# Optimization experiments

Measured on AMD Instinct MI355X. Metric: run time of the kernel, lower is better.

Reference implementation:

```python
import jax, jax.numpy as jnp
import numpy as np

EMBED_DIM = 1024
NUM_HEADS = 16
HEAD_DIM = EMBED_DIM // NUM_HEADS
B, S = 2, 2048


def setup_inputs() -> dict:
    key = jax.random.key(0)
    ks = jax.random.split(key, 8)
    std = 1.0 / np.sqrt(EMBED_DIM)
    return {
        "xq": jax.random.normal(ks[0], (B, S, EMBED_DIM), jnp.float32),
        "xk": jax.random.normal(ks[1], (B, S, EMBED_DIM), jnp.float32),
        "xv": jax.random.normal(ks[2], (B, S, EMBED_DIM), jnp.float32),
        "Wq": jax.random.normal(ks[3], (EMBED_DIM, EMBED_DIM), jnp.float32) * std,
        "Wk": jax.random.normal(ks[4], (EMBED_DIM, EMBED_DIM), jnp.float32) * std,
        "Wv": jax.random.normal(ks[5], (EMBED_DIM, EMBED_DIM), jnp.float32) * std,
        "Wo": jax.random.normal(ks[6], (EMBED_DIM, EMBED_DIM), jnp.float32) * std,
        "bo": jnp.zeros((EMBED_DIM,), jnp.float32),
    }


def reference(xq, xk, xv, Wq, Wk, Wv, Wo, bo):
    # nn.Linear(x) = x @ W.T ; then view last dim into (heads, head_dim)
    def proj(x, W):
        y = jnp.einsum('bse,fe->bsf', x, W)
        return y.reshape(x.shape[0], x.shape[1], NUM_HEADS, HEAD_DIM)

    q = proj(xq, Wq)  # [b, m, h, f]
    k = proj(xk, Wk)  # [b, n, h, f]
    v = proj(xv, Wv)  # [b, n, h, f]

    scaling = 1.0 / np.sqrt(HEAD_DIM).astype(np.float32)
    dot = scaling * jnp.einsum('bmhf,bnhf->bhmn', q, k)  # [b, h, m, n]
    attn = jax.nn.softmax(dot, axis=-1)
    out = jnp.einsum('bhmn,bnhf->bmhf', attn, v)  # [b, m, h, f]

    Wo_hf = Wo.reshape(EMBED_DIM, NUM_HEADS, HEAD_DIM)
    return jnp.einsum('bmhf,ehf->bme', out, Wo_hf) + bo
```

## Files before the change

kernel.cpp:

```cpp
#include <hip/hip_runtime.h>
#include <math.h>


#define EMBED 1024
#define SEQ   2048
#define BATCH 2
#define NH    16
#define HD    64

typedef __attribute__((ext_vector_type(8))) short bf16x8;
typedef __attribute__((ext_vector_type(4))) short bf16x4;
typedef __attribute__((ext_vector_type(4))) float f32x4;

#define QSCALE 0.18033688f

__device__ inline unsigned short f2bf(float f) {
  unsigned int u = __builtin_bit_cast(unsigned int, f);
  u += 0x7fffu + ((u >> 16) & 1u);
  return (unsigned short)(u >> 16);
}
__device__ inline float bf2f(unsigned short s) {
  unsigned int u = ((unsigned int)s) << 16;
  return __builtin_bit_cast(float, u);
}

__device__ inline void async_cp16(const void* g, void* l) {
  __builtin_amdgcn_global_load_lds(
      (const __attribute__((address_space(1))) unsigned int*)g,
      (__attribute__((address_space(3))) unsigned int*)l, 16, 0, 0);
}

__global__ void detect_kernel(const unsigned int* __restrict__ xq, int* __restrict__ flag) {
  __shared__ int cnt[256];
  int t = threadIdx.x;
  unsigned int w = xq[t];
  unsigned int e = (w >> 7) & 0xFFu;
  cnt[t] = (e >= 0x70u && e <= 0x8Fu) ? 1 : 0;
  __syncthreads();
  for (int s = 128; s > 0; s >>= 1) {
    if (t < s) cnt[t] += cnt[t + s];
    __syncthreads();
  }
  if (t == 0) *flag = (cnt[0] >= 160) ? 1 : 0;
}

struct PackPtrs {
  const void* src[7];
  unsigned short* dst[7];
};
__global__ __launch_bounds__(256) void pack_all(PackPtrs p, const int* __restrict__ flagp) {
  const bool isbf = (*flagp != 0);
  int ci = blockIdx.x * 256 + threadIdx.x;
  int t, rel;
  if (ci < 1572864) { t = ci / 524288; rel = ci - t * 524288; }
  else { int r = ci - 1572864; int w = r / 131072; t = 3 + w; rel = r - w * 131072; }
  size_t off = (size_t)rel * 8;
  unsigned short* d = p.dst[t] + off;
  if (isbf) {
    *(bf16x8*)d = *(const bf16x8*)((const unsigned short*)p.src[t] + off);
  } else {
    const float* s = (const float*)p.src[t] + off;
    bf16x8 v;
#pragma unroll
    for (int e = 0; e < 8; ++e) v[e] = (short)f2bf(s[e]);
    *(bf16x8*)d = v;
  }
}

struct QkvArgs {
  const unsigned short* A[3];
  const unsigned short* W[3];
  unsigned short* out[3];
};
__global__ __launch_bounds__(256) void gemm_qkv(QkvArgs args) {
  __shared__ __align__(16) unsigned short smem[16640];
  unsigned short* As = smem;
  unsigned short* Bs = smem + 4096;

  const int z = blockIdx.z;
  const unsigned short* A = args.A[z];
  const unsigned short* Bw = args.W[z];
  unsigned short* out = args.out[z];

  const int tid = threadIdx.x, lane = tid & 63, wave = tid >> 6;
  const int wm = wave >> 1, wn = wave & 1;
  const int q = lane >> 4, c = lane & 15;
  const int m0 = blockIdx.x * 128, n0 = blockIdx.y * 128;

  f32x4 acc[4][4];
#pragma unroll
  for (int i = 0; i < 4; ++i)
#pragma unroll
    for (int j = 0; j < 4; ++j) acc[i][j] = (f32x4){0.f, 0.f, 0.f, 0.f};

  for (int k0 = 0; k0 < EMBED; k0 += 32) {
    __syncthreads();
#pragma unroll
    for (int jj = 0; jj < 2; ++jj) {
      int ci = jj * 256 + tid;
      async_cp16(A + (size_t)(m0 + (ci >> 2)) * EMBED + k0 + (ci & 3) * 8,
                 (void*)(As + (jj * 256 + wave * 64) * 8));
      async_cp16(Bw + (size_t)(n0 + (ci >> 2)) * EMBED + k0 + (ci & 3) * 8,
                 (void*)(Bs + (jj * 256 + wave * 64) * 8));
    }
    __syncthreads();

    bf16x8 af[4], bfr[4];
#pragma unroll
    for (int i = 0; i < 4; ++i)
      af[i] = *(const bf16x8*)(As + (wm * 64 + i * 16 + c) * 32 + q * 8);
#pragma unroll
    for (int j = 0; j < 4; ++j)
      bfr[j] = *(const bf16x8*)(Bs + (wn * 64 + j * 16 + c) * 32 + q * 8);
#pragma unroll
    for (int i = 0; i < 4; ++i)
#pragma unroll
      for (int j = 0; j < 4; ++j)
        acc[i][j] = __builtin_amdgcn_mfma_f32_16x16x32_bf16(af[i], bfr[j], acc[i][j], 0, 0, 0);
  }

  if (z < 2) {
    const float sc = (z == 0) ? QSCALE : 1.0f;
#pragma unroll
    for (int i = 0; i < 4; ++i)
#pragma unroll
      for (int j = 0; j < 4; ++j)
#pragma unroll
        for (int r = 0; r < 4; ++r) {
          int m = m0 + wm * 64 + i * 16 + q * 4 + r;
          int col = n0 + wn * 64 + j * 16 + c;
          int b = m >> 11, s = m & 2047, h = col >> 6, d = col & 63;
          out[(size_t)((b * NH + h) * SEQ + s) * HD + d] = f2bf(acc[i][j][r] * sc);
        }
  } else {
    __syncthreads();
#pragma unroll
    for (int i = 0; i < 4; ++i)
#pragma unroll
      for (int j = 0; j < 4; ++j)
#pragma unroll
        for (int r = 0; r < 4; ++r)
          smem[(wm * 64 + i * 16 + q * 4 + r) * 130 + wn * 64 + j * 16 + c] =
              f2bf(acc[i][j][r]);
    __syncthreads();
    int n = tid >> 1;
    int sh = (tid & 1) * 64;
    int b = m0 >> 11, s0l = m0 & 2047;
    int h = blockIdx.y * 2 + (n >> 6), d = n & 63;
    unsigned short* dst = out + (size_t)((b * NH + h) * HD + d) * SEQ + s0l + sh;
#pragma unroll
    for (int g = 0; g < 8; ++g) {
      bf16x8 v;
#pragma unroll
      for (int e = 0; e < 8; ++e) v[e] = (short)smem[(sh + g * 8 + e) * 130 + n];
      *(bf16x8*)(dst + g * 8) = v;
    }
  }
}

__global__ __launch_bounds__(256) void gemm_out(
    const unsigned short* __restrict__ A,
    const unsigned short* __restrict__ Bw,
    const void* __restrict__ bias,
    void* __restrict__ out,
    const int* __restrict__ flagp)
{
  __shared__ __align__(16) unsigned short As[4096];
  __shared__ __align__(16) unsigned short Bs[4096];

  const int tid = threadIdx.x, lane = tid & 63, wave = tid >> 6;
  const int wm = wave >> 1, wn = wave & 1;
  const int q = lane >> 4, c = lane & 15;
  const int m0 = blockIdx.x * 128, n0 = blockIdx.y * 128;

  f32x4 acc[4][4];
#pragma unroll
  for (int i = 0; i < 4; ++i)
#pragma unroll
    for (int j = 0; j < 4; ++j) acc[i][j] = (f32x4){0.f, 0.f, 0.f, 0.f};

  for (int k0 = 0; k0 < EMBED; k0 += 32) {
    __syncthreads();
#pragma unroll
    for (int jj = 0; jj < 2; ++jj) {
      int ci = jj * 256 + tid;
      async_cp16(A + (size_t)(m0 + (ci >> 2)) * EMBED + k0 + (ci & 3) * 8,
                 (void*)(As + (jj * 256 + wave * 64) * 8));
      async_cp16(Bw + (size_t)(n0 + (ci >> 2)) * EMBED + k0 + (ci & 3) * 8,
                 (void*)(Bs + (jj * 256 + wave * 64) * 8));
    }
    __syncthreads();

    bf16x8 af[4], bfr[4];
#pragma unroll
    for (int i = 0; i < 4; ++i)
      af[i] = *(const bf16x8*)(As + (wm * 64 + i * 16 + c) * 32 + q * 8);
#pragma unroll
    for (int j = 0; j < 4; ++j)
      bfr[j] = *(const bf16x8*)(Bs + (wn * 64 + j * 16 + c) * 32 + q * 8);
#pragma unroll
    for (int i = 0; i < 4; ++i)
#pragma unroll
      for (int j = 0; j < 4; ++j)
        acc[i][j] = __builtin_amdgcn_mfma_f32_16x16x32_bf16(af[i], bfr[j], acc[i][j], 0, 0, 0);
  }

  const bool isbf = (*flagp != 0);
#pragma unroll
  for (int i = 0; i < 4; ++i)
#pragma unroll
    for (int j = 0; j < 4; ++j)
#pragma unroll
      for (int r = 0; r < 4; ++r) {
        int m = m0 + wm * 64 + i * 16 + q * 4 + r;
        int col = n0 + wn * 64 + j * 16 + c;
        float v = acc[i][j][r];
        v += isbf ? bf2f(((const unsigned short*)bias)[col]) : ((const float*)bias)[col];
        if (isnan(v)) v = 777.0f;
        if (isbf) ((unsigned short*)out)[(size_t)m * EMBED + col] = f2bf(v);
        else      ((float*)out)[(size_t)m * EMBED + col] = v;
      }
}

__global__ __launch_bounds__(256) void attn_kernel(
    const unsigned short* __restrict__ Qb,
    const unsigned short* __restrict__ Kb,
    const unsigned short* __restrict__ Vtb,
    unsigned short* __restrict__ Ob)
{
  __shared__ __align__(16) unsigned short Kt[2][64][72];
  __shared__ __align__(16) unsigned short Vs[2][64][72];

  const int tid = threadIdx.x;
  const int lane = tid & 63;
  const int wave = tid >> 6;
  const int q = lane >> 4, c = lane & 15;
  const int b = blockIdx.z, h = blockIdx.y;
  const int q0 = blockIdx.x * 64 + wave * 16;

  const unsigned short* Qh = Qb + ((size_t)(b * NH + h) * SEQ) * HD;
  const unsigned short* Kh = Kb + ((size_t)(b * NH + h) * SEQ) * HD;
  const unsigned short* Vh = Vtb + ((size_t)(b * NH + h) * HD) * SEQ;

  bf16x8 qfl = *(const bf16x8*)(Qh + (q0 + c) * HD + q * 8);
  bf16x8 qfh = *(const bf16x8*)(Qh + (q0 + c) * HD + 32 + q * 8);

  f32x4 o[4];
#pragma unroll
  for (int t = 0; t < 4; ++t) o[t] = (f32x4){0.f, 0.f, 0.f, 0.f};
  float l = 0.f;

  const int r0 = tid >> 3;
  const int ch0 = (tid & 7) * 8;

  bf16x8 kr0, kr1, vr0, vr1;
  kr0 = *(const bf16x8*)(Kh + (size_t)r0 * HD + ch0);
  kr1 = *(const bf16x8*)(Kh + (size_t)(32 + r0) * HD + ch0);
  vr0 = *(const bf16x8*)(Vh + (size_t)r0 * SEQ + ch0);
  vr1 = *(const bf16x8*)(Vh + (size_t)(32 + r0) * SEQ + ch0);
  *(bf16x8*)(&Kt[0][r0][ch0]) = kr0;
  *(bf16x8*)(&Kt[0][32 + r0][ch0]) = kr1;
  *(bf16x8*)(&Vs[0][r0][ch0]) = vr0;
  *(bf16x8*)(&Vs[0][32 + r0][ch0]) = vr1;

  for (int kt = 0; kt < SEQ / 64; ++kt) {
    const int p = kt & 1;
    __syncthreads();
    if (kt + 1 < SEQ / 64) {
      kr0 = *(const bf16x8*)(Kh + (size_t)((kt + 1) * 64 + r0) * HD + ch0);
      kr1 = *(const bf16x8*)(Kh + (size_t)((kt + 1) * 64 + 32 + r0) * HD + ch0);
      vr0 = *(const bf16x8*)(Vh + (size_t)r0 * SEQ + (kt + 1) * 64 + ch0);
      vr1 = *(const bf16x8*)(Vh + (size_t)(32 + r0) * SEQ + (kt + 1) * 64 + ch0);
    }

#pragma unroll
    for (int g = 0; g < 2; ++g) {
      bf16x4 pk[2];
#pragma unroll
      for (int s2 = 0; s2 < 2; ++s2) {
        const int s = g * 2 + s2;
        bf16x8 k0f = *(const bf16x8*)(&Kt[p][s * 16 + c][q * 8]);
        bf16x8 k1f = *(const bf16x8*)(&Kt[p][s * 16 + c][32 + q * 8]);
        f32x4 z = {0.f, 0.f, 0.f, 0.f};
        z = __builtin_amdgcn_mfma_f32_16x16x32_bf16(k0f, qfl, z, 0, 0, 0);
        z = __builtin_amdgcn_mfma_f32_16x16x32_bf16(k1f, qfh, z, 0, 0, 0);
#pragma unroll
        for (int r = 0; r < 4; ++r) {
          float pv = __builtin_amdgcn_exp2f(z[r]);
          l += pv;
          pk[s2][r] = (short)(__builtin_bit_cast(unsigned int, pv) >> 16);
        }
      }
#pragma unroll
      for (int t = 0; t < 4; ++t) {
        bf16x4 v0 = *(const bf16x4*)(&Vs[p][t * 16 + c][g * 32 + q * 4]);
        bf16x4 v1 = *(const bf16x4*)(&Vs[p][t * 16 + c][g * 32 + 16 + q * 4]);
        bf16x8 vf, pf;
#pragma unroll
        for (int e = 0; e < 4; ++e) {
          vf[e] = v0[e]; vf[4 + e] = v1[e];
          pf[e] = pk[0][e]; pf[4 + e] = pk[1][e];
        }
        o[t] = __builtin_amdgcn_mfma_f32_16x16x32_bf16(pf, vf, o[t], 0, 0, 0);
      }
    }

    if (kt + 1 < SEQ / 64) {
      *(bf16x8*)(&Kt[1 - p][r0][ch0]) = kr0;
      *(bf16x8*)(&Kt[1 - p][32 + r0][ch0]) = kr1;
      *(bf16x8*)(&Vs[1 - p][r0][ch0]) = vr0;
      *(bf16x8*)(&Vs[1 - p][32 + r0][ch0]) = vr1;
    }
  }

  float ls = l;
  ls += __shfl_xor(ls, 16);
  ls += __shfl_xor(ls, 32);
  float lf[4];
#pragma unroll
  for (int r = 0; r < 4; ++r) lf[r] = 1.f / __shfl(ls, q * 4 + r);
#pragma unroll
  for (int t = 0; t < 4; ++t)
#pragma unroll
    for (int r = 0; r < 4; ++r) {
      int srow = q0 + q * 4 + r;
      int col = h * HD + t * 16 + c;
      float val = o[t][r] * lf[r];
      if (isnan(val)) val = 77.0f;
      Ob[((size_t)(b * SEQ + srow)) * EMBED + col] = f2bf(val);
    }
}

__device__ inline bf16x8 load8(const void* p, int idx, bool isbf) {
  if (isbf) return *(const bf16x8*)((const unsigned short*)p + idx);
  const float* f = (const float*)p + idx;
  bf16x8 r;
#pragma unroll
  for (int i = 0; i < 8; ++i) r[i] = (short)f2bf(f[i]);
  return r;
}
__global__ __launch_bounds__(256) void gemm_bt(
    const void* __restrict__ A, const void* __restrict__ Bw,
    const void* __restrict__ bias, void* __restrict__ out,
    const int* __restrict__ flagp, int mode, float scale)
{
  const bool isbf = (*flagp != 0);
  const bool a_isbf = isbf || (mode == 0);
  const int lane = threadIdx.x & 63;
  const int wave = threadIdx.x >> 6;
  const int tile = blockIdx.x * 4 + wave;
  const int mt = tile >> 4, nt = tile & 15;
  const int q = lane >> 4, c = lane & 15;
  const int m0 = mt * 16, n0 = nt * 64;

  f32x4 acc[4];
#pragma unroll
  for (int t = 0; t < 4; ++t) acc[t] = (f32x4){0.f, 0.f, 0.f, 0.f};

  for (int k0 = 0; k0 < EMBED; k0 += 32) {
    bf16x8 a = load8(A, (m0 + c) * EMBED + k0 + q * 8, a_isbf);
#pragma unroll
    for (int t = 0; t < 4; ++t) {
      bf16x8 b = load8(Bw, (n0 + t * 16 + c) * EMBED + k0 + q * 8, isbf);
      acc[t] = __builtin_amdgcn_mfma_f32_16x16x32_bf16(a, b, acc[t], 0, 0, 0);
    }
  }
#pragma unroll
  for (int t = 0; t < 4; ++t)
#pragma unroll
    for (int r = 0; r < 4; ++r) {
      float v = acc[t][r] * scale;
      int row = m0 + q * 4 + r, col = n0 + t * 16 + c;
      if (mode == 0) {
        v += isbf ? bf2f(((const unsigned short*)bias)[col]) : ((const float*)bias)[col];
        if (isbf) ((unsigned short*)out)[row * EMBED + col] = f2bf(v);
        else      ((float*)out)[row * EMBED + col] = v;
      } else {
        int b = row >> 11, s = row & 2047, h = col >> 6, d = col & 63;
        if (mode == 1) ((unsigned short*)out)[(((b * NH + h) * SEQ) + s) * HD + d] = f2bf(v);
        else           ((unsigned short*)out)[(((b * NH + h) * HD) + d) * SEQ + s] = f2bf(v);
      }
    }
}

extern "C" void kernel_launch(void* const* d_in, const int* in_sizes, int n_in,
                              void* d_out, int out_size, void* d_ws, size_t ws_size,
                              hipStream_t stream) {
  const void* xq = d_in[0]; const void* xk = d_in[1]; const void* xv = d_in[2];
  const void* Wq = d_in[3]; const void* Wk = d_in[4]; const void* Wv = d_in[5];
  const void* Wo = d_in[6]; const void* bo = d_in[7];

  const size_t NEL = (size_t)BATCH * SEQ * EMBED;
  const size_t WEL = (size_t)EMBED * EMBED;
  unsigned short* base = (unsigned short*)d_ws;

  unsigned short* Xq = base;
  unsigned short* Xk = Xq + NEL;
  unsigned short* Xv = Xk + NEL;
  unsigned short* Wqb = Xv + NEL;
  unsigned short* Wkb = Wqb + WEL;
  unsigned short* Wvb = Wkb + WEL;
  unsigned short* Wob = Wvb + WEL;
  unsigned short* Q  = Wob + WEL;
  unsigned short* K  = Q + NEL;
  unsigned short* Vt = K + NEL;
  unsigned short* AO = Xq;
  int* flagF = (int*)(Vt + NEL);
  size_t need = ((char*)(flagF + 16)) - (char*)d_ws;

  if (ws_size >= need) {
    detect_kernel<<<1, 256, 0, stream>>>((const unsigned int*)xq, flagF);
    PackPtrs pp;
    pp.src[0] = xq; pp.src[1] = xk; pp.src[2] = xv;
    pp.src[3] = Wq; pp.src[4] = Wk; pp.src[5] = Wv; pp.src[6] = Wo;
    pp.dst[0] = Xq; pp.dst[1] = Xk; pp.dst[2] = Xv;
    pp.dst[3] = Wqb; pp.dst[4] = Wkb; pp.dst[5] = Wvb; pp.dst[6] = Wob;
    pack_all<<<8192, 256, 0, stream>>>(pp, flagF);

    QkvArgs qa;
    qa.A[0] = Xq; qa.A[1] = Xk; qa.A[2] = Xv;
    qa.W[0] = Wqb; qa.W[1] = Wkb; qa.W[2] = Wvb;
    qa.out[0] = Q; qa.out[1] = K; qa.out[2] = Vt;
    gemm_qkv<<<dim3(32, 8, 3), 256, 0, stream>>>(qa);
    attn_kernel<<<dim3(32, NH, BATCH), 256, 0, stream>>>(Q, K, Vt, AO);
    gemm_out<<<dim3(32, 8), 256, 0, stream>>>(AO, Wob, bo, d_out, flagF);
  } else {
    unsigned short* Qf  = base;
    unsigned short* Kf  = Qf + NEL;
    unsigned short* Vtf = Kf + NEL;
    unsigned short* AOf = Vtf + NEL;
    int* flag = (int*)(AOf + NEL);
    detect_kernel<<<1, 256, 0, stream>>>((const unsigned int*)xq, flag);
    dim3 gblk(1024, 1, 1);
    gemm_bt<<<gblk, 256, 0, stream>>>(xq, Wq, nullptr, Qf, flag, 1, QSCALE);
    gemm_bt<<<gblk, 256, 0, stream>>>(xk, Wk, nullptr, Kf, flag, 1, 1.0f);
    gemm_bt<<<gblk, 256, 0, stream>>>(xv, Wv, nullptr, Vtf, flag, 2, 1.0f);
    attn_kernel<<<dim3(32, NH, BATCH), 256, 0, stream>>>(Qf, Kf, Vtf, AOf);
    gemm_bt<<<gblk, 256, 0, stream>>>(AOf, Wo, bo, d_out, flag, 0, 1.0f);
  }
}
```

Before: 254.8 us.

## Drop dtype detection, widen GEMM K-tiles with XOR swizzle, load V directly in attention

Removes the bf16/f32 detection kernel and all runtime dtype branches, so inputs are always treated as fp32. The QKV and output GEMMs now stage K-tiles of 64 instead of 32, with an XOR-swizzled LDS layout to avoid bank conflicts. The output GEMM uses 64-row tiles for more blocks. Attention drops the V shared-memory staging: V^T is stored pre-permuted so MFMA operands come straight from global memory, and occupancy is hinted via launch bounds. This trades fewer syncs and less LDS for more global-load latency in the attention loop and tighter coupling between the V writer and reader layouts.

```diff
diff --git a/kernel.cpp b/kernel.cpp
--- a/kernel.cpp
+++ b/kernel.cpp
@@ -19,10 +19,6 @@
   u += 0x7fffu + ((u >> 16) & 1u);
   return (unsigned short)(u >> 16);
 }
-__device__ inline float bf2f(unsigned short s) {
-  unsigned int u = ((unsigned int)s) << 16;
-  return __builtin_bit_cast(float, u);
-}
 
 __device__ inline void async_cp16(const void* g, void* l) {
   __builtin_amdgcn_global_load_lds(
@@ -30,41 +26,28 @@
       (__attribute__((address_space(3))) unsigned int*)l, 16, 0, 0);
 }
 
-__global__ void detect_kernel(const unsigned int* __restrict__ xq, int* __restrict__ flag) {
-  __shared__ int cnt[256];
-  int t = threadIdx.x;
-  unsigned int w = xq[t];
-  unsigned int e = (w >> 7) & 0xFFu;
-  cnt[t] = (e >= 0x70u && e <= 0x8Fu) ? 1 : 0;
-  __syncthreads();
-  for (int s = 128; s > 0; s >>= 1) {
-    if (t < s) cnt[t] += cnt[t + s];
-    __syncthreads();
-  }
-  if (t == 0) *flag = (cnt[0] >= 160) ? 1 : 0;
+__device__ inline int vswz_src(int p) {
+  return (p & ~31) + 16 * ((p >> 2) & 1) + 4 * ((p >> 3) & 3) + (p & 3);
+}
+__device__ inline int vswz_pos(int s) {
+  return (s & ~31) + 8 * ((s >> 2) & 3) + 4 * ((s >> 4) & 1) + (s & 3);
 }
 
 struct PackPtrs {
-  const void* src[7];
+  const float* src[7];
   unsigned short* dst[7];
 };
-__global__ __launch_bounds__(256) void pack_all(PackPtrs p, const int* __restrict__ flagp) {
-  const bool isbf = (*flagp != 0);
+__global__ __launch_bounds__(256) void pack_all(PackPtrs p) {
   int ci = blockIdx.x * 256 + threadIdx.x;
   int t, rel;
   if (ci < 1572864) { t = ci / 524288; rel = ci - t * 524288; }
   else { int r = ci - 1572864; int w = r / 131072; t = 3 + w; rel = r - w * 131072; }
   size_t off = (size_t)rel * 8;
-  unsigned short* d = p.dst[t] + off;
-  if (isbf) {
-    *(bf16x8*)d = *(const bf16x8*)((const unsigned short*)p.src[t] + off);
-  } else {
-    const float* s = (const float*)p.src[t] + off;
-    bf16x8 v;
-#pragma unroll
-    for (int e = 0; e < 8; ++e) v[e] = (short)f2bf(s[e]);
-    *(bf16x8*)d = v;
-  }
+  const float* s = p.src[t] + off;
+  bf16x8 v;
+#pragma unroll
+  for (int e = 0; e < 8; ++e) v[e] = (short)f2bf(s[e]);
+  *(bf16x8*)(p.dst[t] + off) = v;
 }
 
 struct QkvArgs {
@@ -75,7 +58,7 @@
 __global__ __launch_bounds__(256) void gemm_qkv(QkvArgs args) {
   __shared__ __align__(16) unsigned short smem[16640];
   unsigned short* As = smem;
-  unsigned short* Bs = smem + 4096;
+  unsigned short* Bs = smem + 8192;
 
   const int z = blockIdx.z;
   const unsigned short* A = args.A[z];
@@ -93,30 +76,36 @@
 #pragma unroll
     for (int j = 0; j < 4; ++j) acc[i][j] = (f32x4){0.f, 0.f, 0.f, 0.f};
 
-  for (int k0 = 0; k0 < EMBED; k0 += 32) {
-    __syncthreads();
-#pragma unroll
-    for (int jj = 0; jj < 2; ++jj) {
+  for (int k0 = 0; k0 < EMBED; k0 += 64) {
+    __syncthreads();
+#pragma unroll
+    for (int jj = 0; jj < 4; ++jj) {
       int ci = jj * 256 + tid;
-      async_cp16(A + (size_t)(m0 + (ci >> 2)) * EMBED + k0 + (ci & 3) * 8,
+      int row = ci >> 3, sc = ((ci & 7) ^ (row & 7)) * 8;
+      async_cp16(A + (size_t)(m0 + row) * EMBED + k0 + sc,
                  (void*)(As + (jj * 256 + wave * 64) * 8));
-      async_cp16(Bw + (size_t)(n0 + (ci >> 2)) * EMBED + k0 + (ci & 3) * 8,
+      async_cp16(Bw + (size_t)(n0 + row) * EMBED + k0 + sc,
                  (void*)(Bs + (jj * 256 + wave * 64) * 8));
     }
     __syncthreads();
 
-    bf16x8 af[4], bfr[4];
-#pragma unroll
-    for (int i = 0; i < 4; ++i)
-      af[i] = *(const bf16x8*)(As + (wm * 64 + i * 16 + c) * 32 + q * 8);
-#pragma unroll
-    for (int j = 0; j < 4; ++j)
-      bfr[j] = *(const bf16x8*)(Bs + (wn * 64 + j * 16 + c) * 32 + q * 8);
-#pragma unroll
-    for (int i = 0; i < 4; ++i)
+#pragma unroll
+    for (int kk = 0; kk < 2; ++kk) {
+      bf16x8 af[4], bfr[4];
+#pragma unroll
+      for (int i = 0; i < 4; ++i)
+        af[i] = *(const bf16x8*)(As + (wm * 64 + i * 16 + c) * 64 +
+                                 (((kk * 4 + q) ^ (c & 7)) * 8));
 #pragma unroll
       for (int j = 0; j < 4; ++j)
-        acc[i][j] = __builtin_amdgcn_mfma_f32_16x16x32_bf16(af[i], bfr[j], acc[i][j], 0, 0, 0);
+        bfr[j] = *(const bf16x8*)(Bs + (wn * 64 + j * 16 + c) * 64 +
+                                  (((kk * 4 + q) ^ (c & 7)) * 8));
+#pragma unroll
+      for (int i = 0; i < 4; ++i)
+#pragma unroll
+        for (int j = 0; j < 4; ++j)
+          acc[i][j] = __builtin_amdgcn_mfma_f32_16x16x32_bf16(af[i], bfr[j], acc[i][j], 0, 0, 0);
+    }
   }
 
   if (z < 2) {
@@ -152,7 +141,8 @@
     for (int g = 0; g < 8; ++g) {
       bf16x8 v;
 #pragma unroll
-      for (int e = 0; e < 8; ++e) v[e] = (short)smem[(sh + g * 8 + e) * 130 + n];
+      for (int e = 0; e < 8; ++e)
+        v[e] = (short)smem[vswz_src(sh + g * 8 + e) * 130 + n];
       *(bf16x8*)(dst + g * 8) = v;
     }
   }
@@ -161,75 +151,81 @@
 __global__ __launch_bounds__(256) void gemm_out(
     const unsigned short* __restrict__ A,
     const unsigned short* __restrict__ Bw,
-    const void* __restrict__ bias,
-    void* __restrict__ out,
-    const int* __restrict__ flagp)
+    const float* __restrict__ bias,
+    float* __restrict__ out)
 {
   __shared__ __align__(16) unsigned short As[4096];
-  __shared__ __align__(16) unsigned short Bs[4096];
+  __shared__ __align__(16) unsigned short Bs[8192];
 
   const int tid = threadIdx.x, lane = tid & 63, wave = tid >> 6;
   const int wm = wave >> 1, wn = wave & 1;
   const int q = lane >> 4, c = lane & 15;
-  const int m0 = blockIdx.x * 128, n0 = blockIdx.y * 128;
-
-  f32x4 acc[4][4];
-#pragma unroll
-  for (int i = 0; i < 4; ++i)
+  const int m0 = blockIdx.x * 64, n0 = blockIdx.y * 128;
+
+  f32x4 acc[2][4];
+#pragma unroll
+  for (int i = 0; i < 2; ++i)
 #pragma unroll
     for (int j = 0; j < 4; ++j) acc[i][j] = (f32x4){0.f, 0.f, 0.f, 0.f};
 
-  for (int k0 = 0; k0 < EMBED; k0 += 32) {
+  for (int k0 = 0; k0 < EMBED; k0 += 64) {
     __syncthreads();
 #pragma unroll
     for (int jj = 0; jj < 2; ++jj) {
       int ci = jj * 256 + tid;
-      async_cp16(A + (size_t)(m0 + (ci >> 2)) * EMBED + k0 + (ci & 3) * 8,
+      int row = ci >> 3, sc = ((ci & 7) ^ (row & 7)) * 8;
+      async_cp16(A + (size_t)(m0 + row) * EMBED + k0 + sc,
                  (void*)(As + (jj * 256 + wave * 64) * 8));
-      async_cp16(Bw + (size_t)(n0 + (ci >> 2)) * EMBED + k0 + (ci & 3) * 8,
+    }
+#pragma unroll
+    for (int jj = 0; jj < 4; ++jj) {
+      int ci = jj * 256 + tid;
+      int row = ci >> 3, sc = ((ci & 7) ^ (row & 7)) * 8;
+      async_cp16(Bw + (size_t)(n0 + row) * EMBED + k0 + sc,
                  (void*)(Bs + (jj * 256 + wave * 64) * 8));
     }
     __syncthreads();
 
-    bf16x8 af[4], bfr[4];
-#pragma unroll
-    for (int i = 0; i < 4; ++i)
-      af[i] = *(const bf16x8*)(As + (wm * 64 + i * 16 + c) * 32 + q * 8);
+#pragma unroll
+    for (int kk = 0; kk < 2; ++kk) {
+      bf16x8 af[2], bfr[4];
+#pragma unroll
+      for (int i = 0; i < 2; ++i)
+        af[i] = *(const bf16x8*)(As + (wm * 32 + i * 16 + c) * 64 +
+                                 (((kk * 4 + q) ^ (c & 7)) * 8));
+#pragma unroll
+      for (int j = 0; j < 4; ++j)
+        bfr[j] = *(const bf16x8*)(Bs + (wn * 64 + j * 16 + c) * 64 +
+                                  (((kk * 4 + q) ^ (c & 7)) * 8));
+#pragma unroll
+      for (int i = 0; i < 2; ++i)
+#pragma unroll
+        for (int j = 0; j < 4; ++j)
+          acc[i][j] = __builtin_amdgcn_mfma_f32_16x16x32_bf16(af[i], bfr[j], acc[i][j], 0, 0, 0);
+    }
+  }
+
+#pragma unroll
+  for (int i = 0; i < 2; ++i)
 #pragma unroll
     for (int j = 0; j < 4; ++j)
-      bfr[j] = *(const bf16x8*)(Bs + (wn * 64 + j * 16 + c) * 32 + q * 8);
-#pragma unroll
-    for (int i = 0; i < 4; ++i)
-#pragma unroll
-      for (int j = 0; j < 4; ++j)
-        acc[i][j] = __builtin_amdgcn_mfma_f32_16x16x32_bf16(af[i], bfr[j], acc[i][j], 0, 0, 0);
-  }
-
-  const bool isbf = (*flagp != 0);
-#pragma unroll
-  for (int i = 0; i < 4; ++i)
-#pragma unroll
-    for (int j = 0; j < 4; ++j)
 #pragma unroll
       for (int r = 0; r < 4; ++r) {
-        int m = m0 + wm * 64 + i * 16 + q * 4 + r;
+        int m = m0 + wm * 32 + i * 16 + q * 4 + r;
         int col = n0 + wn * 64 + j * 16 + c;
-        float v = acc[i][j][r];
-        v += isbf ? bf2f(((const unsigned short*)bias)[col]) : ((const float*)bias)[col];
+        float v = acc[i][j][r] + bias[col];
         if (isnan(v)) v = 777.0f;
-        if (isbf) ((unsigned short*)out)[(size_t)m * EMBED + col] = f2bf(v);
-        else      ((float*)out)[(size_t)m * EMBED + col] = v;
+        out[(size_t)m * EMBED + col] = v;
       }
 }
 
-__global__ __launch_bounds__(256) void attn_kernel(
+__global__ __launch_bounds__(256, 4) void attn_kernel(
     const unsigned short* __restrict__ Qb,
     const unsigned short* __restrict__ Kb,
     const unsigned short* __restrict__ Vtb,
     unsigned short* __restrict__ Ob)
 {
   __shared__ __align__(16) unsigned short Kt[2][64][72];
-  __shared__ __align__(16) unsigned short Vs[2][64][72];
 
   const int tid = threadIdx.x;
   const int lane = tid & 63;
@@ -253,15 +249,11 @@
   const int r0 = tid >> 3;
   const int ch0 = (tid & 7) * 8;
 
-  bf16x8 kr0, kr1, vr0, vr1;
+  bf16x8 kr0, kr1;
   kr0 = *(const bf16x8*)(Kh + (size_t)r0 * HD + ch0);
   kr1 = *(const bf16x8*)(Kh + (size_t)(32 + r0) * HD + ch0);
-  vr0 = *(const bf16x8*)(Vh + (size_t)r0 * SEQ + ch0);
-  vr1 = *(const bf16x8*)(Vh + (size_t)(32 + r0) * SEQ + ch0);
   *(bf16x8*)(&Kt[0][r0][ch0]) = kr0;
   *(bf16x8*)(&Kt[0][32 + r0][ch0]) = kr1;
-  *(bf16x8*)(&Vs[0][r0][ch0]) = vr0;
-  *(bf16x8*)(&Vs[0][32 + r0][ch0]) = vr1;
 
   for (int kt = 0; kt < SEQ / 64; ++kt) {
     const int p = kt & 1;
@@ -269,9 +261,14 @@
     if (kt + 1 < SEQ / 64) {
       kr0 = *(const bf16x8*)(Kh + (size_t)((kt + 1) * 64 + r0) * HD + ch0);
       kr1 = *(const bf16x8*)(Kh + (size_t)((kt + 1) * 64 + 32 + r0) * HD + ch0);
-      vr0 = *(const bf16x8*)(Vh + (size_t)r0 * SEQ + (kt + 1) * 64 + ch0);
-      vr1 = *(const bf16x8*)(Vh + (size_t)(32 + r0) * SEQ + (kt + 1) * 64 + ch0);
-    }
+    }
+    bf16x8 vb[4][2];
+#pragma unroll
+    for (int t = 0; t < 4; ++t)
+#pragma unroll
+      for (int g = 0; g < 2; ++g)
+        vb[t][g] = *(const bf16x8*)(Vh + (size_t)(t * 16 + c) * SEQ +
+                                    kt * 64 + g * 32 + q * 8);
 
 #pragma unroll
     for (int g = 0; g < 2; ++g) {
@@ -293,23 +290,16 @@
       }
 #pragma unroll
       for (int t = 0; t < 4; ++t) {
-        bf16x4 v0 = *(const bf16x4*)(&Vs[p][t * 16 + c][g * 32 + q * 4]);
-        bf16x4 v1 = *(const bf16x4*)(&Vs[p][t * 16 + c][g * 32 + 16 + q * 4]);
-        bf16x8 vf, pf;
-#pragma unroll
-        for (int e = 0; e < 4; ++e) {
-          vf[e] = v0[e]; vf[4 + e] = v1[e];
-          pf[e] = pk[0][e]; pf[4 + e] = pk[1][e];
-        }
-        o[t] = __builtin_amdgcn_mfma_f32_16x16x32_bf16(pf, vf, o[t], 0, 0, 0);
+        bf16x8 pf;
+#pragma unroll
+        for (int e = 0; e < 4; ++e) { pf[e] = pk[0][e]; pf[4 + e] = pk[1][e]; }
+        o[t] = __builtin_amdgcn_mfma_f32_16x16x32_bf16(pf, vb[t][g], o[t], 0, 0, 0);
       }
     }
 
     if (kt + 1 < SEQ / 64) {
       *(bf16x8*)(&Kt[1 - p][r0][ch0]) = kr0;
       *(bf16x8*)(&Kt[1 - p][32 + r0][ch0]) = kr1;
-      *(bf16x8*)(&Vs[1 - p][r0][ch0]) = vr0;
-      *(bf16x8*)(&Vs[1 - p][32 + r0][ch0]) = vr1;
     }
   }
 
@@ -331,9 +321,7 @@
     }
 }
 
-__device__ inline bf16x8 load8(const void* p, int idx, bool isbf) {
-  if (isbf) return *(const bf16x8*)((const unsigned short*)p + idx);
-  const float* f = (const float*)p + idx;
+__device__ inline bf16x8 load8f(const float* f) {
   bf16x8 r;
 #pragma unroll
   for (int i = 0; i < 8; ++i) r[i] = (short)f2bf(f[i]);
@@ -341,11 +329,9 @@
 }
 __global__ __launch_bounds__(256) void gemm_bt(
     const void* __restrict__ A, const void* __restrict__ Bw,
-    const void* __restrict__ bias, void* __restrict__ out,
-    const int* __restrict__ flagp, int mode, float scale)
+    const float* __restrict__ bias, void* __restrict__ out,
+    int mode, float scale)
 {
-  const bool isbf = (*flagp != 0);
-  const bool a_isbf = isbf || (mode == 0);
   const int lane = threadIdx.x & 63;
   const int wave = threadIdx.x >> 6;
   const int tile = blockIdx.x * 4 + wave;
@@ -358,10 +344,12 @@
   for (int t = 0; t < 4; ++t) acc[t] = (f32x4){0.f, 0.f, 0.f, 0.f};
 
   for (int k0 = 0; k0 < EMBED; k0 += 32) {
-    bf16x8 a = load8(A, (m0 + c) * EMBED + k0 + q * 8, a_isbf);
+    bf16x8 a = (mode == 0)
+        ? *(const bf16x8*)((const unsigned short*)A + (m0 + c) * EMBED + k0 + q * 8)
+        : load8f((const float*)A + (m0 + c) * EMBED + k0 + q * 8);
 #pragma unroll
     for (int t = 0; t < 4; ++t) {
-      bf16x8 b = load8(Bw, (n0 + t * 16 + c) * EMBED + k0 + q * 8, isbf);
+      bf16x8 b = load8f((const float*)Bw + (size_t)(n0 + t * 16 + c) * EMBED + k0 + q * 8);
       acc[t] = __builtin_amdgcn_mfma_f32_16x16x32_bf16(a, b, acc[t], 0, 0, 0);
     }
   }
@@ -372,13 +360,14 @@
       float v = acc[t][r] * scale;
       int row = m0 + q * 4 + r, col = n0 + t * 16 + c;
       if (mode == 0) {
-        v += isbf ? bf2f(((const unsigned short*)bias)[col]) : ((const float*)bias)[col];
-        if (isbf) ((unsigned short*)out)[row * EMBED + col] = f2bf(v);
-        else      ((float*)out)[row * EMBED + col] = v;
+        v += bias[col];
+        ((float*)out)[(size_t)row * EMBED + col] = v;
       } else {
         int b = row >> 11, s = row & 2047, h = col >> 6, d = col & 63;
-        if (mode == 1) ((unsigned short*)out)[(((b * NH + h) * SEQ) + s) * HD + d] = f2bf(v);
-        else           ((unsigned short*)out)[(((b * NH + h) * HD) + d) * SEQ + s] = f2bf(v);
+        if (mode == 1)
+          ((unsigned short*)out)[(size_t)((b * NH + h) * SEQ + s) * HD + d] = f2bf(v);
+        else
+          ((unsigned short*)out)[(size_t)((b * NH + h) * HD + d) * SEQ + vswz_pos(s)] = f2bf(v);
       }
     }
 }
@@ -386,9 +375,14 @@
 extern "C" void kernel_launch(void* const* d_in, const int* in_sizes, int n_in,
                               void* d_out, int out_size, void* d_ws, size_t ws_size,
                               hipStream_t stream) {
-  const void* xq = d_in[0]; const void* xk = d_in[1]; const void* xv = d_in[2];
-  const void* Wq = d_in[3]; const void* Wk = d_in[4]; const void* Wv = d_in[5];
-  const void* Wo = d_in[6]; const void* bo = d_in[7];
+  const float* xq = (const float*)d_in[0];
+  const float* xk = (const float*)d_in[1];
+  const float* xv = (const float*)d_in[2];
+  const float* Wq = (const float*)d_in[3];
+  const float* Wk = (const float*)d_in[4];
+  const float* Wv = (const float*)d_in[5];
+  const float* Wo = (const float*)d_in[6];
+  const float* bo = (const float*)d_in[7];
 
   const size_t NEL = (size_t)BATCH * SEQ * EMBED;
   const size_t WEL = (size_t)EMBED * EMBED;
@@ -405,17 +399,15 @@
   unsigned short* K  = Q + NEL;
   unsigned short* Vt = K + NEL;
   unsigned short* AO = Xq;
-  int* flagF = (int*)(Vt + NEL);
-  size_t need = ((char*)(flagF + 16)) - (char*)d_ws;
+  size_t need = (size_t)(6 * NEL + 4 * WEL) * sizeof(unsigned short);
 
   if (ws_size >= need) {
-    detect_kernel<<<1, 256, 0, stream>>>((const unsigned int*)xq, flagF);
     PackPtrs pp;
     pp.src[0] = xq; pp.src[1] = xk; pp.src[2] = xv;
     pp.src[3] = Wq; pp.src[4] = Wk; pp.src[5] = Wv; pp.src[6] = Wo;
     pp.dst[0] = Xq; pp.dst[1] = Xk; pp.dst[2] = Xv;
     pp.dst[3] = Wqb; pp.dst[4] = Wkb; pp.dst[5] = Wvb; pp.dst[6] = Wob;
-    pack_all<<<8192, 256, 0, stream>>>(pp, flagF);
+    pack_all<<<8192, 256, 0, stream>>>(pp);
 
     QkvArgs qa;
     qa.A[0] = Xq; qa.A[1] = Xk; qa.A[2] = Xv;
@@ -423,19 +415,17 @@
     qa.out[0] = Q; qa.out[1] = K; qa.out[2] = Vt;
     gemm_qkv<<<dim3(32, 8, 3), 256, 0, stream>>>(qa);
     attn_kernel<<<dim3(32, NH, BATCH), 256, 0, stream>>>(Q, K, Vt, AO);
-    gemm_out<<<dim3(32, 8), 256, 0, stream>>>(AO, Wob, bo, d_out, flagF);
+    gemm_out<<<dim3(64, 8), 256, 0, stream>>>(AO, Wob, bo, (float*)d_out);
   } else {
     unsigned short* Qf  = base;
     unsigned short* Kf  = Qf + NEL;
     unsigned short* Vtf = Kf + NEL;
     unsigned short* AOf = Vtf + NEL;
-    int* flag = (int*)(AOf + NEL);
-    detect_kernel<<<1, 256, 0, stream>>>((const unsigned int*)xq, flag);
     dim3 gblk(1024, 1, 1);
-    gemm_bt<<<gblk, 256, 0, stream>>>(xq, Wq, nullptr, Qf, flag, 1, QSCALE);
-    gemm_bt<<<gblk, 256, 0, stream>>>(xk, Wk, nullptr, Kf, flag, 1, 1.0f);
-    gemm_bt<<<gblk, 256, 0, stream>>>(xv, Wv, nullptr, Vtf, flag, 2, 1.0f);
+    gemm_bt<<<gblk, 256, 0, stream>>>(xq, Wq, nullptr, Qf, 1, QSCALE);
+    gemm_bt<<<gblk, 256, 0, stream>>>(xk, Wk, nullptr, Kf, 1, 1.0f);
+    gemm_bt<<<gblk, 256, 0, stream>>>(xv, Wv, nullptr, Vtf, 2, 1.0f);
     attn_kernel<<<dim3(32, NH, BATCH), 256, 0, stream>>>(Qf, Kf, Vtf, AOf);
-    gemm_bt<<<gblk, 256, 0, stream>>>(AOf, Wo, bo, d_out, flag, 0, 1.0f);
-  }
-}
+    gemm_bt<<<gblk, 256, 0, stream>>>(AOf, Wo, bo, d_out, 0, 1.0f);
+  }
+}
```

After: 294.5 us. +15.6%, slower.
